# Optimization experiments

Measured on AMD Instinct MI355X. Metric: run time of the kernel, lower is better.

Reference implementation:

```python
import jax, jax.numpy as jnp
import numpy as np

KNN = 5
SEARCH = 3
CUTOFF = 1.0
NCLASSES = 21
D, H, W = 32, 128, 2048
P = 1048576


def setup_inputs() -> dict:
    key = jax.random.key(0)
    k1, k2, k3, k4, k5, k6 = jax.random.split(key, 6)
    proj_range = jax.random.uniform(k1, (D, H, W), dtype=jnp.float32)
    unproj_range = jax.random.uniform(k2, (P,), dtype=jnp.float32)
    proj_argmax = jax.random.randint(k3, (D, H, W), 0, NCLASSES).astype(jnp.int32)
    px = jax.random.randint(k4, (P,), 0, W).astype(jnp.int32)
    py = jax.random.randint(k5, (P,), 0, H).astype(jnp.int32)
    pz = jax.random.randint(k6, (P,), 0, D).astype(jnp.int32)
    return {"proj_range": proj_range, "unproj_range": unproj_range,
            "proj_argmax": proj_argmax, "px": px, "py": py, "pz": pz}


def reference(proj_range, unproj_range, proj_argmax, px, py, pz):
    pad = (SEARCH - 1) // 2
    k3 = SEARCH ** 3
    center = (k3 - 1) // 2  # = 13 for search=3
    n_pts = unproj_range.shape[0]

    # zero padding replicates F.unfold's implicit zero pad (padded entries stay 0,
    # which is NOT mapped to inf by the `< 0` mask, matching the torch code)
    pr_pad = jnp.pad(proj_range, pad)
    pa_pad = jnp.pad(proj_argmax, pad)

    # kernel offsets, flattened in (dz, dy, dx) order like unfoldNd
    offs = jnp.arange(SEARCH, dtype=jnp.int32)
    oz, oy, ox = jnp.meshgrid(offs, offs, offs, indexing="ij")
    oz, oy, ox = oz.reshape(-1), oy.reshape(-1), ox.reshape(-1)  # [k3]

    # per-point neighborhood indices into the padded volume: [P, k3]
    zi = pz[:, None] + oz[None, :]
    yi = py[:, None] + oy[None, :]
    xi = px[:, None] + ox[None, :]

    nb_rang = pr_pad[zi, yi, xi]                       # [P, k3]
    nb_rang = jnp.where(nb_rang < 0, jnp.inf, nb_rang)
    nb_rang = nb_rang.at[:, center].set(unproj_range)  # center = query range

    k2_dist = jnp.abs(nb_rang - unproj_range[:, None])  # [P, k3]

    neg_top, knn_idx = jax.lax.top_k(-k2_dist, KNN)     # smallest-k distances
    knn_dist = -neg_top                                  # [P, KNN]

    nb_arg = pa_pad[zi, yi, xi]                          # [P, k3] int
    knn_arg = jnp.take_along_axis(nb_arg, knn_idx, axis=1)
    knn_arg = jnp.where(knn_dist > CUTOFF, NCLASSES, knn_arg)  # cutoff -> invalid class

    # scatter-add voting over classes 0..NCLASSES
    counts = jnp.zeros((n_pts, NCLASSES + 1), dtype=proj_range.dtype)
    counts = counts.at[jnp.arange(n_pts, dtype=jnp.int32)[:, None], knn_arg].add(1.0)

    # argmax over classes 1..NCLASSES-1 (drop class 0 and invalid bucket), then +1
    out = jnp.argmax(counts[:, 1:-1], axis=1).astype(jnp.int32) + 1
    return out
```

## Files before the change

### kernel.cpp

```cpp
#include <hip/hip_runtime.h>
#include <hip/hip_bf16.h>
#include <math.h>

#define KNN 5
#define K3 27
#define CENTER 13
#define NCLASSES 21
#define DIM_D 32
#define DIM_H 128
#define DIM_W 2048

#define RADIX 256
#define BIN_PTS 2048
#define BIN_THREADS 256

__device__ __forceinline__ unsigned key16(int x, int y, int z) {
    return ((unsigned)z << 11) | ((unsigned)y << 4) | ((unsigned)x >> 7);
}

__global__ __launch_bounds__(256) void hist0_kernel(
    const int* __restrict__ px, const int* __restrict__ py,
    unsigned* __restrict__ h0, int P)
{
    __shared__ unsigned lh0[RADIX];
    int t = threadIdx.x;
    lh0[t] = 0;
    __syncthreads();
    int base4 = blockIdx.x * 1024 + t;
#pragma unroll
    for (int g = 0; g < 4; ++g) {
        int i4 = base4 + g * 256;
        int i0 = i4 * 4;
        if (i0 + 3 < P) {
            int4 X = ((const int4*)px)[i4];
            int4 Y = ((const int4*)py)[i4];
            atomicAdd(&lh0[(((unsigned)Y.x & 0xF) << 4) | ((unsigned)X.x >> 7)], 1u);
            atomicAdd(&lh0[(((unsigned)Y.y & 0xF) << 4) | ((unsigned)X.y >> 7)], 1u);
            atomicAdd(&lh0[(((unsigned)Y.z & 0xF) << 4) | ((unsigned)X.z >> 7)], 1u);
            atomicAdd(&lh0[(((unsigned)Y.w & 0xF) << 4) | ((unsigned)X.w >> 7)], 1u);
        } else {
            for (int i = i0; i < P; ++i)
                atomicAdd(&lh0[(((unsigned)py[i] & 0xF) << 4) | ((unsigned)px[i] >> 7)], 1u);
        }
    }
    __syncthreads();
    if (lh0[t]) atomicAdd(&h0[t], lh0[t]);
}

__global__ __launch_bounds__(256) void scan256_kernel(unsigned* __restrict__ h)
{
    __shared__ unsigned ws[4];
    int t = threadIdx.x, lane = t & 63, wid = t >> 6;
    unsigned a = h[t], ia = a;
#pragma unroll
    for (int off = 1; off < 64; off <<= 1) {
        unsigned v = __shfl_up(ia, off);
        if (lane >= off) ia += v;
    }
    if (lane == 63) ws[wid] = ia;
    __syncthreads();
    unsigned b = 0;
#pragma unroll
    for (int w = 0; w < 4; ++w) b += (w < wid) ? ws[w] : 0u;
    h[t] = b + ia - a;
}

struct BinShared {
    unsigned lh[RADIX];
    unsigned lscan[RADIX];
    unsigned gbase[RADIX];
    unsigned wsum[4];
    uint4 stage[BIN_PTS];
};

__device__ __forceinline__ void bin_local_scan(BinShared& S, int t)
{
    int lane = t & 63, wid = t >> 6;
    unsigned c = S.lh[t];
    unsigned inc = c;
#pragma unroll
    for (int off = 1; off < 64; off <<= 1) {
        unsigned v = __shfl_up(inc, off);
        if (lane >= off) inc += v;
    }
    if (lane == 63) S.wsum[wid] = inc;
    __syncthreads();
    unsigned wb = 0;
#pragma unroll
    for (int w = 0; w < 4; ++w) wb += (w < wid) ? S.wsum[w] : 0u;
    S.lscan[t] = wb + inc - c;
}

__global__ __launch_bounds__(BIN_THREADS) void bin_pass1_kernel(
    const float* __restrict__ ur, const int* __restrict__ px,
    const int* __restrict__ py, const int* __restrict__ pz,
    unsigned* __restrict__ g0, uint4* __restrict__ outp, int P)
{
    __shared__ BinShared S;
    int t = threadIdx.x;
    int bstart = blockIdx.x * BIN_PTS;
    int n = min(BIN_PTS, P - bstart);
    S.lh[t] = 0;
    __syncthreads();

    uint4 pay[8];
    unsigned rk[8], dg[8];
#pragma unroll
    for (int g = 0; g < 2; ++g) {
        int i4 = (bstart >> 2) + g * 256 + t;
        int i0 = i4 * 4;
        if (i0 + 3 < P) {
            int4 X = ((const int4*)px)[i4];
            int4 Y = ((const int4*)py)[i4];
            int4 Z = ((const int4*)pz)[i4];
            float4 U = ((const float4*)ur)[i4];
            int xs[4] = {X.x, X.y, X.z, X.w};
            int ys[4] = {Y.x, Y.y, Y.z, Y.w};
            int zs[4] = {Z.x, Z.y, Z.z, Z.w};
            float us[4] = {U.x, U.y, U.z, U.w};
#pragma unroll
            for (int c = 0; c < 4; ++c) {
                int j = g * 4 + c;
                unsigned k = key16(xs[c], ys[c], zs[c]);
                dg[j] = k & 0xFFu;
                rk[j] = atomicAdd(&S.lh[dg[j]], 1u);
                pay[j] = make_uint4(__float_as_uint(us[c]),
                    (unsigned)xs[c] | ((unsigned)ys[c] << 11) | ((unsigned)zs[c] << 18),
                    (unsigned)(i0 + c), 0u);
            }
        } else {
#pragma unroll
            for (int c = 0; c < 4; ++c) {
                int j = g * 4 + c;
                int gi = i0 + c;
                if (gi < P) {
                    int x = px[gi], y = py[gi], z = pz[gi];
                    unsigned k = key16(x, y, z);
                    dg[j] = k & 0xFFu;
                    rk[j] = atomicAdd(&S.lh[dg[j]], 1u);
                    pay[j] = make_uint4(__float_as_uint(ur[gi]),
                        (unsigned)x | ((unsigned)y << 11) | ((unsigned)z << 18),
                        (unsigned)gi, 0u);
                } else {
                    dg[j] = 0xFFFFFFFFu;
                }
            }
        }
    }
    __syncthreads();
    bin_local_scan(S, t);
    S.gbase[t] = S.lh[t] ? atomicAdd(&g0[t], S.lh[t]) : 0u;
    __syncthreads();
#pragma unroll
    for (int j = 0; j < 8; ++j)
        if (dg[j] != 0xFFFFFFFFu)
            S.stage[S.lscan[dg[j]] + rk[j]] = pay[j];
    __syncthreads();
#pragma unroll
    for (int j = 0; j < 8; ++j) {
        int s = j * 256 + t;
        if (s < n) {
            uint4 v = S.stage[s];
            unsigned d = (v.y >> 7) & 0xFFu;
            unsigned pos = S.gbase[d] + ((unsigned)s - S.lscan[d]);
            outp[pos] = v;
        }
    }
}

__global__ __launch_bounds__(BIN_THREADS) void hist_p2_kernel(
    const uint4* __restrict__ inp, unsigned* __restrict__ M,
    int gridB, int P)
{
    __shared__ unsigned lh[RADIX];
    int t = threadIdx.x;
    lh[t] = 0;
    __syncthreads();
    int bstart = blockIdx.x * BIN_PTS;
#pragma unroll
    for (int j = 0; j < 8; ++j) {
        int i = bstart + j * 256 + t;
        if (i < P) {
            uint4 v = inp[i];
            atomicAdd(&lh[(v.y >> 15) & 0xFFu], 1u);
        }
    }
    __syncthreads();
    M[(unsigned)t * (unsigned)gridB + blockIdx.x] = lh[t];
}

__global__ __launch_bounds__(1024) void scan_digit_kernel(
    unsigned* __restrict__ M, unsigned* __restrict__ T, int gridB)
{
    __shared__ unsigned wsum[16];
    unsigned* row = M + (size_t)blockIdx.x * (unsigned)gridB;
    int t = threadIdx.x, lane = t & 63, wid = t >> 6;
    int C = (gridB + 1023) / 1024;
    int lo = t * C, hi = min(lo + C, gridB);

    unsigned s = 0;
    for (int i = lo; i < hi; ++i) s += row[i];
    unsigned incl = s;
#pragma unroll
    for (int off = 1; off < 64; off <<= 1) {
        unsigned v = __shfl_up(incl, off);
        if (lane >= off) incl += v;
    }
    if (lane == 63) wsum[wid] = incl;
    __syncthreads();
    if (wid == 0 && lane < 16) {
        unsigned v = wsum[lane], iv = v;
#pragma unroll
        for (int off = 1; off < 16; off <<= 1) {
            unsigned u = __shfl_up(iv, off);
            if (lane >= off) iv += u;
        }
        wsum[lane] = iv - v;
    }
    __syncthreads();
    unsigned run = wsum[wid] + (incl - s);
    for (int i = lo; i < hi; ++i) {
        unsigned v = row[i];
        row[i] = run;
        run += v;
    }
    if (t == 1023) T[blockIdx.x] = run;
}

__global__ __launch_bounds__(BIN_THREADS) void bin_pass2_stable_kernel(
    const uint4* __restrict__ inp, const unsigned* __restrict__ M,
    const unsigned* __restrict__ T, uint4* __restrict__ outp,
    int gridB, int P)
{
    __shared__ BinShared S;
    int t = threadIdx.x;
    int bstart = blockIdx.x * BIN_PTS;
    int n = min(BIN_PTS, P - bstart);
    S.lh[t] = 0;
    __syncthreads();

    uint4 pay[8];
    unsigned rk[8], dg[8];
#pragma unroll
    for (int j = 0; j < 8; ++j) {
        int i = bstart + j * 256 + t;
        if (i < P) {
            uint4 v = inp[i];
            pay[j] = v;
            dg[j] = (v.y >> 15) & 0xFFu;
            rk[j] = atomicAdd(&S.lh[dg[j]], 1u);
        } else {
            dg[j] = 0xFFFFFFFFu;
        }
    }
    __syncthreads();
    bin_local_scan(S, t);
    S.gbase[t] = T[t] + M[(unsigned)t * (unsigned)gridB + blockIdx.x];
    __syncthreads();
#pragma unroll
    for (int j = 0; j < 8; ++j)
        if (dg[j] != 0xFFFFFFFFu)
            S.stage[S.lscan[dg[j]] + rk[j]] = pay[j];
    __syncthreads();
#pragma unroll
    for (int j = 0; j < 8; ++j) {
        int s = j * 256 + t;
        if (s < n) {
            uint4 v = S.stage[s];
            unsigned d = (v.y >> 15) & 0xFFu;
            unsigned pos = S.gbase[d] + ((unsigned)s - S.lscan[d]);
            outp[pos] = v;
        }
    }
}

__device__ __forceinline__ void bev_knn_body(
    const float* __restrict__ pr, const int* __restrict__ pa,
    float u, int x, int y, int z, int oidx, int* __restrict__ out)
{
    float dist[K3];
#pragma unroll
    for (int k = 0; k < K3; ++k) {
        const int dz = k / 9 - 1;
        const int dy = (k / 3) % 3 - 1;
        const int dx = k % 3 - 1;
        int zz = z + dz, yy = y + dy, xx = x + dx;
        bool ok = ((unsigned)zz < (unsigned)DIM_D) &
                  ((unsigned)yy < (unsigned)DIM_H) &
                  ((unsigned)xx < (unsigned)DIM_W);
        int zi = ok ? zz : 0;
        int yi = ok ? yy : 0;
        int xi = ok ? xx : 0;
        float r = pr[((size_t)zi * DIM_H + yi) * DIM_W + xi];
        r = ok ? r : 0.0f;
        r = (r < 0.0f) ? INFINITY : r;
        float d = fabsf(r - u);
        dist[k] = (k == CENTER) ? 0.0f : d;
    }

    float bd[KNN];
    int   bk[KNN];
#pragma unroll
    for (int j = 0; j < KNN; ++j) { bd[j] = INFINITY; bk[j] = -1; }
#pragma unroll
    for (int k = 0; k < K3; ++k) {
        float dcur = dist[k];
        int   kcur = k;
#pragma unroll
        for (int j = 0; j < KNN; ++j) {
            bool take = dcur < bd[j];
            float td = bd[j]; int tk = bk[j];
            bd[j] = take ? dcur : bd[j];
            bk[j] = take ? kcur : bk[j];
            dcur  = take ? td : dcur;
            kcur  = take ? tk : kcur;
        }
    }

    int votes[KNN];
#pragma unroll
    for (int j = 0; j < KNN; ++j) {
        int k = bk[j];
        const int dz = k / 9 - 1;
        const int dy = (k / 3) % 3 - 1;
        const int dx = k % 3 - 1;
        int zz = z + dz, yy = y + dy, xx = x + dx;
        bool ok = ((unsigned)zz < (unsigned)DIM_D) &
                  ((unsigned)yy < (unsigned)DIM_H) &
                  ((unsigned)xx < (unsigned)DIM_W);
        int zi = ok ? zz : 0;
        int yi = ok ? yy : 0;
        int xi = ok ? xx : 0;
        int cls = pa[((size_t)zi * DIM_H + yi) * DIM_W + xi];
        cls = ok ? cls : 0;
        cls = (bd[j] > 1.0f) ? NCLASSES : cls;
        votes[j] = cls;
    }

    int best_cnt = 0, best_cls = 1;
#pragma unroll
    for (int j = 0; j < KNN; ++j) {
        int v = votes[j];
        if (v >= 1 && v <= NCLASSES - 1) {
            int cnt = 0;
#pragma unroll
            for (int i = 0; i < KNN; ++i) cnt += (votes[i] == v) ? 1 : 0;
            if (cnt > best_cnt || (cnt == best_cnt && v < best_cls)) {
                best_cnt = cnt;
                best_cls = v;
            }
        }
    }
    out[oidx] = best_cls;
}

__device__ __forceinline__ int swizzle_block(int b, int nb) {
    if ((nb & 7) == 0) {
        int per = nb >> 3;
        return (b & 7) * per + (b >> 3);
    }
    return b;
}

__global__ __launch_bounds__(256) void bev_knn_aos_kernel(
    const float* __restrict__ pr, const int* __restrict__ pa,
    const uint4* __restrict__ payload, int* __restrict__ out, int P)
{
    int lb = swizzle_block(blockIdx.x, gridDim.x);
    int p = lb * blockDim.x + threadIdx.x;
    if (p >= P) return;
    uint4 w = payload[p];
    float u = __uint_as_float(w.x);
    int x = (int)(w.y & 0x7FFu);
    int y = (int)((w.y >> 11) & 0x7Fu);
    int z = (int)((w.y >> 18) & 0x1Fu);
    bev_knn_body(pr, pa, u, x, y, z, (int)w.z, out);
}

__global__ __launch_bounds__(256) void bev_knn_direct_kernel(
    const float* __restrict__ pr, const int* __restrict__ pa,
    const float* __restrict__ ur, const int* __restrict__ px,
    const int* __restrict__ py, const int* __restrict__ pz,
    int* __restrict__ out, int P)
{
    int p = blockIdx.x * blockDim.x + threadIdx.x;
    if (p >= P) return;
    bev_knn_body(pr, pa, ur[p], px[p], py[p], pz[p], p, out);
}

extern "C" void kernel_launch(void* const* d_in, const int* in_sizes, int n_in,
                              void* d_out, int out_size, void* d_ws, size_t ws_size,
                              hipStream_t stream) {
    const float* pr = (const float*)d_in[0];
    const float* ur = (const float*)d_in[1];
    const int*   pa = (const int*)d_in[2];
    const int*   px = (const int*)d_in[3];
    const int*   py = (const int*)d_in[4];
    const int*   pz = (const int*)d_in[5];
    int* out = (int*)d_out;
    int P = in_sizes[1];
    int block = 256;
    int grid = (P + block - 1) / block;
    int gridH = (P + 4095) / 4096;
    int gridB = (P + BIN_PTS - 1) / BIN_PTS;

    size_t h_b   = (size_t)RADIX * 4;
    size_t t_b   = (size_t)RADIX * 4;
    size_t m_b   = (size_t)RADIX * (size_t)gridB * 4;
    size_t m_off = (h_b + t_b + m_b + 15) & ~(size_t)15;
    size_t pay_b = (size_t)P * 16;
    size_t need_stable = m_off + 2 * pay_b;

    if (ws_size >= need_stable) {
        char* ws = (char*)d_ws;
        unsigned* h0   = (unsigned*)ws;
        unsigned* T    = (unsigned*)(ws + h_b);
        unsigned* M    = (unsigned*)(ws + h_b + t_b);
        uint4*    pay1 = (uint4*)(ws + m_off);
        uint4*    pay2 = (uint4*)(ws + m_off + pay_b);

        hipMemsetAsync(h0, 0, h_b, stream);
        hist0_kernel<<<gridH, 256, 0, stream>>>(px, py, h0, P);
        scan256_kernel<<<1, 256, 0, stream>>>(h0);
        bin_pass1_kernel<<<gridB, BIN_THREADS, 0, stream>>>(ur, px, py, pz,
                                                            h0, pay1, P);
        hist_p2_kernel<<<gridB, BIN_THREADS, 0, stream>>>(pay1, M, gridB, P);
        scan_digit_kernel<<<RADIX, 1024, 0, stream>>>(M, T, gridB);
        scan256_kernel<<<1, 256, 0, stream>>>(T);
        bin_pass2_stable_kernel<<<gridB, BIN_THREADS, 0, stream>>>(
            pay1, M, T, pay2, gridB, P);
        bev_knn_aos_kernel<<<grid, block, 0, stream>>>(pr, pa, pay2, out, P);
    } else {
        bev_knn_direct_kernel<<<grid, block, 0, stream>>>(pr, pa, ur, px, py,
                                                          pz, out, P);
    }
}
```

Before: 203.1 us.

## Fuse pass-2 histogram into pass-1 scatter and process two points per thread

Drops the separate hist_p2 kernel. Pass 1 now builds the second-digit per-block histogram M directly with global atomics keyed by destination block (pos>>11), and M is zeroed by an enlarged memset. The KNN kernel is also rewritten to handle two points per thread, interleaving their 27 gathers to raise memory-level parallelism, with half as many blocks. The costs are global atomic contention on M and higher register pressure from doubling per-thread state.

```diff
diff --git a/kernel.cpp b/kernel.cpp
--- a/kernel.cpp
+++ b/kernel.cpp
@@ -94,7 +94,8 @@
 __global__ __launch_bounds__(BIN_THREADS) void bin_pass1_kernel(
     const float* __restrict__ ur, const int* __restrict__ px,
     const int* __restrict__ py, const int* __restrict__ pz,
-    unsigned* __restrict__ g0, uint4* __restrict__ outp, int P)
+    unsigned* __restrict__ g0, uint4* __restrict__ outp,
+    unsigned* __restrict__ M, int gridB, int P)
 {
     __shared__ BinShared S;
     int t = threadIdx.x;
@@ -164,29 +165,10 @@
             unsigned d = (v.y >> 7) & 0xFFu;
             unsigned pos = S.gbase[d] + ((unsigned)s - S.lscan[d]);
             outp[pos] = v;
-        }
-    }
-}
-
-__global__ __launch_bounds__(BIN_THREADS) void hist_p2_kernel(
-    const uint4* __restrict__ inp, unsigned* __restrict__ M,
-    int gridB, int P)
-{
-    __shared__ unsigned lh[RADIX];
-    int t = threadIdx.x;
-    lh[t] = 0;
-    __syncthreads();
-    int bstart = blockIdx.x * BIN_PTS;
-#pragma unroll
-    for (int j = 0; j < 8; ++j) {
-        int i = bstart + j * 256 + t;
-        if (i < P) {
-            uint4 v = inp[i];
-            atomicAdd(&lh[(v.y >> 15) & 0xFFu], 1u);
-        }
-    }
-    __syncthreads();
-    M[(unsigned)t * (unsigned)gridB + blockIdx.x] = lh[t];
+            unsigned d1 = (v.y >> 15) & 0xFFu;
+            atomicAdd(&M[d1 * (unsigned)gridB + (pos >> 11)], 1u);
+        }
+    }
 }
 
 __global__ __launch_bounds__(1024) void scan_digit_kernel(
@@ -274,10 +256,134 @@
     }
 }
 
-__device__ __forceinline__ void bev_knn_body(
+__device__ __forceinline__ int swizzle_block(int b, int nb) {
+    if ((nb & 7) == 0) {
+        int per = nb >> 3;
+        return (b & 7) * per + (b >> 3);
+    }
+    return b;
+}
+
+__global__ __launch_bounds__(256) void bev_knn_aos2_kernel(
     const float* __restrict__ pr, const int* __restrict__ pa,
-    float u, int x, int y, int z, int oidx, int* __restrict__ out)
-{
+    const uint4* __restrict__ payload, int* __restrict__ out, int P)
+{
+    int lb = swizzle_block(blockIdx.x, gridDim.x);
+    int t = threadIdx.x;
+    int idx[2] = { lb * 512 + t, lb * 512 + 256 + t };
+
+    bool act[2];
+    float u[2];
+    int x[2], y[2], z[2], oidx[2];
+#pragma unroll
+    for (int q = 0; q < 2; ++q) {
+        act[q] = idx[q] < P;
+        uint4 w = payload[act[q] ? idx[q] : 0];
+        u[q] = __uint_as_float(w.x);
+        x[q] = (int)(w.y & 0x7FFu);
+        y[q] = (int)((w.y >> 11) & 0x7Fu);
+        z[q] = (int)((w.y >> 18) & 0x1Fu);
+        oidx[q] = (int)w.z;
+    }
+
+    float dist[2][K3];
+#pragma unroll
+    for (int k = 0; k < K3; ++k) {
+        const int dz = k / 9 - 1;
+        const int dy = (k / 3) % 3 - 1;
+        const int dx = k % 3 - 1;
+#pragma unroll
+        for (int q = 0; q < 2; ++q) {
+            int zz = z[q] + dz, yy = y[q] + dy, xx = x[q] + dx;
+            bool ok = ((unsigned)zz < (unsigned)DIM_D) &
+                      ((unsigned)yy < (unsigned)DIM_H) &
+                      ((unsigned)xx < (unsigned)DIM_W);
+            int zi = ok ? zz : 0;
+            int yi = ok ? yy : 0;
+            int xi = ok ? xx : 0;
+            float r = pr[((size_t)zi * DIM_H + yi) * DIM_W + xi];
+            r = ok ? r : 0.0f;
+            r = (r < 0.0f) ? INFINITY : r;
+            float d = fabsf(r - u[q]);
+            dist[q][k] = (k == CENTER) ? 0.0f : d;
+        }
+    }
+
+    float bd[2][KNN];
+    int   bk[2][KNN];
+#pragma unroll
+    for (int q = 0; q < 2; ++q) {
+#pragma unroll
+        for (int j = 0; j < KNN; ++j) { bd[q][j] = INFINITY; bk[q][j] = -1; }
+#pragma unroll
+        for (int k = 0; k < K3; ++k) {
+            float dcur = dist[q][k];
+            int   kcur = k;
+#pragma unroll
+            for (int j = 0; j < KNN; ++j) {
+                bool take = dcur < bd[q][j];
+                float td = bd[q][j]; int tk = bk[q][j];
+                bd[q][j] = take ? dcur : bd[q][j];
+                bk[q][j] = take ? kcur : bk[q][j];
+                dcur = take ? td : dcur;
+                kcur = take ? tk : kcur;
+            }
+        }
+    }
+
+    int votes[2][KNN];
+#pragma unroll
+    for (int j = 0; j < KNN; ++j) {
+#pragma unroll
+        for (int q = 0; q < 2; ++q) {
+            int k = bk[q][j];
+            const int dz = k / 9 - 1;
+            const int dy = (k / 3) % 3 - 1;
+            const int dx = k % 3 - 1;
+            int zz = z[q] + dz, yy = y[q] + dy, xx = x[q] + dx;
+            bool ok = ((unsigned)zz < (unsigned)DIM_D) &
+                      ((unsigned)yy < (unsigned)DIM_H) &
+                      ((unsigned)xx < (unsigned)DIM_W);
+            int zi = ok ? zz : 0;
+            int yi = ok ? yy : 0;
+            int xi = ok ? xx : 0;
+            int cls = pa[((size_t)zi * DIM_H + yi) * DIM_W + xi];
+            cls = ok ? cls : 0;
+            cls = (bd[q][j] > 1.0f) ? NCLASSES : cls;
+            votes[q][j] = cls;
+        }
+    }
+
+#pragma unroll
+    for (int q = 0; q < 2; ++q) {
+        int best_cnt = 0, best_cls = 1;
+#pragma unroll
+        for (int j = 0; j < KNN; ++j) {
+            int v = votes[q][j];
+            if (v >= 1 && v <= NCLASSES - 1) {
+                int cnt = 0;
+#pragma unroll
+                for (int i = 0; i < KNN; ++i) cnt += (votes[q][i] == v) ? 1 : 0;
+                if (cnt > best_cnt || (cnt == best_cnt && v < best_cls)) {
+                    best_cnt = cnt;
+                    best_cls = v;
+                }
+            }
+        }
+        if (act[q]) out[oidx[q]] = best_cls;
+    }
+}
+
+__global__ __launch_bounds__(256) void bev_knn_direct_kernel(
+    const float* __restrict__ pr, const int* __restrict__ pa,
+    const float* __restrict__ ur, const int* __restrict__ px,
+    const int* __restrict__ py, const int* __restrict__ pz,
+    int* __restrict__ out, int P)
+{
+    int p = blockIdx.x * blockDim.x + threadIdx.x;
+    if (p >= P) return;
+    float u = ur[p];
+    int x = px[p], y = py[p], z = pz[p];
     float dist[K3];
 #pragma unroll
     for (int k = 0; k < K3; ++k) {
@@ -297,26 +403,22 @@
         float d = fabsf(r - u);
         dist[k] = (k == CENTER) ? 0.0f : d;
     }
-
-    float bd[KNN];
-    int   bk[KNN];
+    float bd[KNN]; int bk[KNN];
 #pragma unroll
     for (int j = 0; j < KNN; ++j) { bd[j] = INFINITY; bk[j] = -1; }
 #pragma unroll
     for (int k = 0; k < K3; ++k) {
-        float dcur = dist[k];
-        int   kcur = k;
+        float dcur = dist[k]; int kcur = k;
 #pragma unroll
         for (int j = 0; j < KNN; ++j) {
             bool take = dcur < bd[j];
             float td = bd[j]; int tk = bk[j];
             bd[j] = take ? dcur : bd[j];
             bk[j] = take ? kcur : bk[j];
-            dcur  = take ? td : dcur;
-            kcur  = take ? tk : kcur;
-        }
-    }
-
+            dcur = take ? td : dcur;
+            kcur = take ? tk : kcur;
+        }
+    }
     int votes[KNN];
 #pragma unroll
     for (int j = 0; j < KNN; ++j) {
@@ -336,7 +438,6 @@
         cls = (bd[j] > 1.0f) ? NCLASSES : cls;
         votes[j] = cls;
     }
-
     int best_cnt = 0, best_cls = 1;
 #pragma unroll
     for (int j = 0; j < KNN; ++j) {
@@ -346,46 +447,11 @@
 #pragma unroll
             for (int i = 0; i < KNN; ++i) cnt += (votes[i] == v) ? 1 : 0;
             if (cnt > best_cnt || (cnt == best_cnt && v < best_cls)) {
-                best_cnt = cnt;
-                best_cls = v;
+                best_cnt = cnt; best_cls = v;
             }
         }
     }
-    out[oidx] = best_cls;
-}
-
-__device__ __forceinline__ int swizzle_block(int b, int nb) {
-    if ((nb & 7) == 0) {
-        int per = nb >> 3;
-        return (b & 7) * per + (b >> 3);
-    }
-    return b;
-}
-
-__global__ __launch_bounds__(256) void bev_knn_aos_kernel(
-    const float* __restrict__ pr, const int* __restrict__ pa,
-    const uint4* __restrict__ payload, int* __restrict__ out, int P)
-{
-    int lb = swizzle_block(blockIdx.x, gridDim.x);
-    int p = lb * blockDim.x + threadIdx.x;
-    if (p >= P) return;
-    uint4 w = payload[p];
-    float u = __uint_as_float(w.x);
-    int x = (int)(w.y & 0x7FFu);
-    int y = (int)((w.y >> 11) & 0x7Fu);
-    int z = (int)((w.y >> 18) & 0x1Fu);
-    bev_knn_body(pr, pa, u, x, y, z, (int)w.z, out);
-}
-
-__global__ __launch_bounds__(256) void bev_knn_direct_kernel(
-    const float* __restrict__ pr, const int* __restrict__ pa,
-    const float* __restrict__ ur, const int* __restrict__ px,
-    const int* __restrict__ py, const int* __restrict__ pz,
-    int* __restrict__ out, int P)
-{
-    int p = blockIdx.x * blockDim.x + threadIdx.x;
-    if (p >= P) return;
-    bev_knn_body(pr, pa, ur[p], px[p], py[p], pz[p], p, out);
+    out[p] = best_cls;
 }
 
 extern "C" void kernel_launch(void* const* d_in, const int* in_sizes, int n_in,
@@ -399,10 +465,9 @@
     const int*   pz = (const int*)d_in[5];
     int* out = (int*)d_out;
     int P = in_sizes[1];
-    int block = 256;
-    int grid = (P + block - 1) / block;
     int gridH = (P + 4095) / 4096;
     int gridB = (P + BIN_PTS - 1) / BIN_PTS;
+    int gridM = (P + 511) / 512;
 
     size_t h_b   = (size_t)RADIX * 4;
     size_t t_b   = (size_t)RADIX * 4;
@@ -419,19 +484,19 @@
         uint4*    pay1 = (uint4*)(ws + m_off);
         uint4*    pay2 = (uint4*)(ws + m_off + pay_b);
 
-        hipMemsetAsync(h0, 0, h_b, stream);
+        hipMemsetAsync(ws, 0, h_b + t_b + m_b, stream);
         hist0_kernel<<<gridH, 256, 0, stream>>>(px, py, h0, P);
         scan256_kernel<<<1, 256, 0, stream>>>(h0);
-        bin_pass1_kernel<<<gridB, BIN_THREADS, 0, stream>>>(ur, px, py, pz,
-                                                            h0, pay1, P);
-        hist_p2_kernel<<<gridB, BIN_THREADS, 0, stream>>>(pay1, M, gridB, P);
+        bin_pass1_kernel<<<gridB, BIN_THREADS, 0, stream>>>(
+            ur, px, py, pz, h0, pay1, M, gridB, P);
         scan_digit_kernel<<<RADIX, 1024, 0, stream>>>(M, T, gridB);
         scan256_kernel<<<1, 256, 0, stream>>>(T);
         bin_pass2_stable_kernel<<<gridB, BIN_THREADS, 0, stream>>>(
             pay1, M, T, pay2, gridB, P);
-        bev_knn_aos_kernel<<<grid, block, 0, stream>>>(pr, pa, pay2, out, P);
+        bev_knn_aos2_kernel<<<gridM, 256, 0, stream>>>(pr, pa, pay2, out, P);
     } else {
-        bev_knn_direct_kernel<<<grid, block, 0, stream>>>(pr, pa, ur, px, py,
-                                                          pz, out, P);
-    }
-}
+        int grid = (P + 255) / 256;
+        bev_knn_direct_kernel<<<grid, 256, 0, stream>>>(pr, pa, ur, px, py,
+                                                        pz, out, P);
+    }
+}
```

Result: slower. 246.2 us (+21.2%).

## Bucket points by (y, x-half, z) segments and stage neighborhood rows in LDS

Applied to the files above, without the earlier changes.

The radix binning now uses segment keys of y plus the x half for its first pass. A per-segment z counting sort replaces the global second-pass histogram, scan and stable scatter, which cuts several kernel launches. The KNN kernel gets one block per (z, y, x-half) segment. Each block loads the 9 neighboring 1024-wide rows of range and packed byte class into LDS, then processes its points from shared memory instead of scattered global gathers. The cost is large per-block LDS use (about 46 KB), uneven work per block, and a pass2 launch of only 256 blocks that loops over whole segments.

```diff
diff --git a/kernel.cpp b/kernel.cpp
--- a/kernel.cpp
+++ b/kernel.cpp
@@ -13,9 +13,16 @@
 #define RADIX 256
 #define BIN_PTS 2048
 #define BIN_THREADS 256
-
-__device__ __forceinline__ unsigned key16(int x, int y, int z) {
-    return ((unsigned)z << 11) | ((unsigned)y << 4) | ((unsigned)x >> 7);
+#define NG 8192
+#define ROWW 1032
+#define SEG_TILE 2048
+
+
+__device__ __forceinline__ unsigned seg_of_xy(int x, int y) {
+    return ((unsigned)y << 1) | ((unsigned)x >> 10);
+}
+__device__ __forceinline__ unsigned seg_of_wy(unsigned wy) {
+    return (((wy >> 11) & 0x7Fu) << 1) | ((wy >> 10) & 1u);
 }
 
 __global__ __launch_bounds__(256) void hist0_kernel(
@@ -34,20 +41,21 @@
         if (i0 + 3 < P) {
             int4 X = ((const int4*)px)[i4];
             int4 Y = ((const int4*)py)[i4];
-            atomicAdd(&lh0[(((unsigned)Y.x & 0xF) << 4) | ((unsigned)X.x >> 7)], 1u);
-            atomicAdd(&lh0[(((unsigned)Y.y & 0xF) << 4) | ((unsigned)X.y >> 7)], 1u);
-            atomicAdd(&lh0[(((unsigned)Y.z & 0xF) << 4) | ((unsigned)X.z >> 7)], 1u);
-            atomicAdd(&lh0[(((unsigned)Y.w & 0xF) << 4) | ((unsigned)X.w >> 7)], 1u);
+            atomicAdd(&lh0[seg_of_xy(X.x, Y.x)], 1u);
+            atomicAdd(&lh0[seg_of_xy(X.y, Y.y)], 1u);
+            atomicAdd(&lh0[seg_of_xy(X.z, Y.z)], 1u);
+            atomicAdd(&lh0[seg_of_xy(X.w, Y.w)], 1u);
         } else {
             for (int i = i0; i < P; ++i)
-                atomicAdd(&lh0[(((unsigned)py[i] & 0xF) << 4) | ((unsigned)px[i] >> 7)], 1u);
+                atomicAdd(&lh0[seg_of_xy(px[i], py[i])], 1u);
         }
     }
     __syncthreads();
     if (lh0[t]) atomicAdd(&h0[t], lh0[t]);
 }
 
-__global__ __launch_bounds__(256) void scan256_kernel(unsigned* __restrict__ h)
+__global__ __launch_bounds__(256) void scan256_dup_kernel(
+    unsigned* __restrict__ h, unsigned* __restrict__ hbase)
 {
     __shared__ unsigned ws[4];
     int t = threadIdx.x, lane = t & 63, wid = t >> 6;
@@ -62,7 +70,9 @@
     unsigned b = 0;
 #pragma unroll
     for (int w = 0; w < 4; ++w) b += (w < wid) ? ws[w] : 0u;
-    h[t] = b + ia - a;
+    unsigned excl = b + ia - a;
+    h[t] = excl;
+    hbase[t] = excl;
 }
 
 struct BinShared {
@@ -121,8 +131,7 @@
 #pragma unroll
             for (int c = 0; c < 4; ++c) {
                 int j = g * 4 + c;
-                unsigned k = key16(xs[c], ys[c], zs[c]);
-                dg[j] = k & 0xFFu;
+                dg[j] = seg_of_xy(xs[c], ys[c]);
                 rk[j] = atomicAdd(&S.lh[dg[j]], 1u);
                 pay[j] = make_uint4(__float_as_uint(us[c]),
                     (unsigned)xs[c] | ((unsigned)ys[c] << 11) | ((unsigned)zs[c] << 18),
@@ -135,8 +144,7 @@
                 int gi = i0 + c;
                 if (gi < P) {
                     int x = px[gi], y = py[gi], z = pz[gi];
-                    unsigned k = key16(x, y, z);
-                    dg[j] = k & 0xFFu;
+                    dg[j] = seg_of_xy(x, y);
                     rk[j] = atomicAdd(&S.lh[dg[j]], 1u);
                     pay[j] = make_uint4(__float_as_uint(ur[gi]),
                         (unsigned)x | ((unsigned)y << 11) | ((unsigned)z << 18),
@@ -161,123 +169,225 @@
         int s = j * 256 + t;
         if (s < n) {
             uint4 v = S.stage[s];
-            unsigned d = (v.y >> 7) & 0xFFu;
+            unsigned d = seg_of_wy(v.y);
             unsigned pos = S.gbase[d] + ((unsigned)s - S.lscan[d]);
             outp[pos] = v;
         }
     }
 }
 
-__global__ __launch_bounds__(BIN_THREADS) void hist_p2_kernel(
-    const uint4* __restrict__ inp, unsigned* __restrict__ M,
-    int gridB, int P)
-{
-    __shared__ unsigned lh[RADIX];
+__global__ __launch_bounds__(256) void pass2z_kernel(
+    const uint4* __restrict__ inp, const unsigned* __restrict__ segBase,
+    uint4* __restrict__ outp, unsigned* __restrict__ st, int P)
+{
+    __shared__ unsigned zh[32];
+    __shared__ unsigned cur[32];
+    __shared__ unsigned lz[32];
+    __shared__ unsigned lsc[32];
+    __shared__ uint4 stage[SEG_TILE];
+
+    int b = blockIdx.x;
+    unsigned s0 = segBase[b];
+    unsigned s1 = (b == RADIX - 1) ? (unsigned)P : segBase[b + 1];
     int t = threadIdx.x;
-    lh[t] = 0;
-    __syncthreads();
-    int bstart = blockIdx.x * BIN_PTS;
-#pragma unroll
-    for (int j = 0; j < 8; ++j) {
-        int i = bstart + j * 256 + t;
-        if (i < P) {
-            uint4 v = inp[i];
-            atomicAdd(&lh[(v.y >> 15) & 0xFFu], 1u);
-        }
-    }
-    __syncthreads();
-    M[(unsigned)t * (unsigned)gridB + blockIdx.x] = lh[t];
-}
-
-__global__ __launch_bounds__(1024) void scan_digit_kernel(
-    unsigned* __restrict__ M, unsigned* __restrict__ T, int gridB)
-{
-    __shared__ unsigned wsum[16];
-    unsigned* row = M + (size_t)blockIdx.x * (unsigned)gridB;
-    int t = threadIdx.x, lane = t & 63, wid = t >> 6;
-    int C = (gridB + 1023) / 1024;
-    int lo = t * C, hi = min(lo + C, gridB);
-
-    unsigned s = 0;
-    for (int i = lo; i < hi; ++i) s += row[i];
-    unsigned incl = s;
-#pragma unroll
-    for (int off = 1; off < 64; off <<= 1) {
-        unsigned v = __shfl_up(incl, off);
-        if (lane >= off) incl += v;
-    }
-    if (lane == 63) wsum[wid] = incl;
-    __syncthreads();
-    if (wid == 0 && lane < 16) {
-        unsigned v = wsum[lane], iv = v;
-#pragma unroll
-        for (int off = 1; off < 16; off <<= 1) {
+
+    if (t < 32) zh[t] = 0;
+    __syncthreads();
+
+    for (unsigned i = s0 + t; i < s1; i += 256)
+        atomicAdd(&zh[(inp[i].y >> 18) & 31u], 1u);
+    __syncthreads();
+
+    if (t < 64) {
+        unsigned v = (t < 32) ? zh[t] : 0u;
+        unsigned iv = v;
+#pragma unroll
+        for (int off = 1; off < 32; off <<= 1) {
             unsigned u = __shfl_up(iv, off);
-            if (lane >= off) iv += u;
-        }
-        wsum[lane] = iv - v;
-    }
-    __syncthreads();
-    unsigned run = wsum[wid] + (incl - s);
-    for (int i = lo; i < hi; ++i) {
-        unsigned v = row[i];
-        row[i] = run;
-        run += v;
-    }
-    if (t == 1023) T[blockIdx.x] = run;
-}
-
-__global__ __launch_bounds__(BIN_THREADS) void bin_pass2_stable_kernel(
-    const uint4* __restrict__ inp, const unsigned* __restrict__ M,
-    const unsigned* __restrict__ T, uint4* __restrict__ outp,
-    int gridB, int P)
-{
-    __shared__ BinShared S;
-    int t = threadIdx.x;
-    int bstart = blockIdx.x * BIN_PTS;
-    int n = min(BIN_PTS, P - bstart);
-    S.lh[t] = 0;
-    __syncthreads();
-
-    uint4 pay[8];
-    unsigned rk[8], dg[8];
-#pragma unroll
-    for (int j = 0; j < 8; ++j) {
-        int i = bstart + j * 256 + t;
-        if (i < P) {
-            uint4 v = inp[i];
-            pay[j] = v;
-            dg[j] = (v.y >> 15) & 0xFFu;
-            rk[j] = atomicAdd(&S.lh[dg[j]], 1u);
-        } else {
-            dg[j] = 0xFFFFFFFFu;
-        }
-    }
-    __syncthreads();
-    bin_local_scan(S, t);
-    S.gbase[t] = T[t] + M[(unsigned)t * (unsigned)gridB + blockIdx.x];
-    __syncthreads();
-#pragma unroll
-    for (int j = 0; j < 8; ++j)
-        if (dg[j] != 0xFFFFFFFFu)
-            S.stage[S.lscan[dg[j]] + rk[j]] = pay[j];
-    __syncthreads();
-#pragma unroll
-    for (int j = 0; j < 8; ++j) {
-        int s = j * 256 + t;
-        if (s < n) {
-            uint4 v = S.stage[s];
-            unsigned d = (v.y >> 15) & 0xFFu;
-            unsigned pos = S.gbase[d] + ((unsigned)s - S.lscan[d]);
-            outp[pos] = v;
-        }
-    }
-}
-
-__device__ __forceinline__ void bev_knn_body(
+            if (t >= off) iv += u;
+        }
+        if (t < 32) {
+            unsigned base = s0 + iv - v;
+            cur[t] = base;
+            st[b * 32 + t] = base;
+        }
+    }
+    __syncthreads();
+
+    for (unsigned tb = s0; tb < s1; tb += SEG_TILE) {
+        unsigned m = min((unsigned)SEG_TILE, s1 - tb);
+        if (t < 32) lz[t] = 0;
+        __syncthreads();
+        uint4 pay[8];
+        unsigned rk[8], zz[8];
+#pragma unroll
+        for (int j = 0; j < 8; ++j) {
+            int s = j * 256 + t;
+            if (s < (int)m) {
+                uint4 v = inp[tb + (unsigned)s];
+                pay[j] = v;
+                zz[j] = (v.y >> 18) & 31u;
+                rk[j] = atomicAdd(&lz[zz[j]], 1u);
+            } else {
+                zz[j] = 0xFFFFFFFFu;
+            }
+        }
+        __syncthreads();
+        if (t < 64) {
+            unsigned v = (t < 32) ? lz[t] : 0u;
+            unsigned iv = v;
+#pragma unroll
+            for (int off = 1; off < 32; off <<= 1) {
+                unsigned u = __shfl_up(iv, off);
+                if (t >= off) iv += u;
+            }
+            if (t < 32) lsc[t] = iv - v;
+        }
+        __syncthreads();
+#pragma unroll
+        for (int j = 0; j < 8; ++j)
+            if (zz[j] != 0xFFFFFFFFu)
+                stage[lsc[zz[j]] + rk[j]] = pay[j];
+        __syncthreads();
+#pragma unroll
+        for (int j = 0; j < 8; ++j) {
+            int s = j * 256 + t;
+            if (s < (int)m) {
+                uint4 v = stage[s];
+                unsigned z = (v.y >> 18) & 31u;
+                outp[cur[z] + ((unsigned)s - lsc[z])] = v;
+            }
+        }
+        __syncthreads();
+        if (t < 32) cur[t] += lz[t];
+        __syncthreads();
+    }
+}
+
+__device__ __forceinline__ int swizzle_block(int b, int nb) {
+    if ((nb & 7) == 0) {
+        int per = nb >> 3;
+        return (b & 7) * per + (b >> 3);
+    }
+    return b;
+}
+
+__global__ __launch_bounds__(256) void bev_knn_lds_kernel(
     const float* __restrict__ pr, const int* __restrict__ pa,
-    float u, int x, int y, int z, int oidx, int* __restrict__ out)
-{
+    const uint4* __restrict__ payload, const unsigned* __restrict__ st,
+    int* __restrict__ out, int P)
+{
+    __shared__ float prs[9 * ROWW];
+    __shared__ unsigned char pas[9 * ROWW];
+
+    int lb = swizzle_block(blockIdx.x, gridDim.x);
+    unsigned start = st[lb];
+    unsigned end   = (lb == NG - 1) ? (unsigned)P : st[lb + 1];
+    int cnt = (int)end - (int)start;
+    if (cnt <= 0) return;
+
+    int y  = lb >> 6;
+    int x0 = ((lb >> 5) & 1) << 10;
+    int z  = lb & 31;
+    int t  = threadIdx.x;
+
+    for (int r = 0; r < 9; ++r) {
+        int gz = z + r / 3 - 1;
+        int gy = y + r % 3 - 1;
+        bool inb = ((unsigned)gz < (unsigned)DIM_D) &
+                   ((unsigned)gy < (unsigned)DIM_H);
+        size_t rb = ((size_t)(gz * DIM_H + gy) << 11) + x0;
+        float4 f = make_float4(0.f, 0.f, 0.f, 0.f);
+        unsigned pk = 0u;
+        if (inb) {
+            f = ((const float4*)(pr + rb))[t];
+            int4 a = ((const int4*)(pa + rb))[t];
+            pk = (unsigned)a.x | ((unsigned)a.y << 8) |
+                 ((unsigned)a.z << 16) | ((unsigned)a.w << 24);
+        }
+        ((float4*)(prs + r * ROWW + 4))[t] = f;
+        ((unsigned*)(pas + r * ROWW + 4))[t] = pk;
+        if (t == 0) {
+            bool okl = inb && (x0 > 0);
+            prs[r * ROWW + 3] = okl ? pr[rb - 1] : 0.f;
+            pas[r * ROWW + 3] = okl ? (unsigned char)pa[rb - 1] : (unsigned char)0;
+            bool okr = inb && (x0 + 1024 < DIM_W);
+            prs[r * ROWW + 1028] = okr ? pr[rb + 1024] : 0.f;
+            pas[r * ROWW + 1028] = okr ? (unsigned char)pa[rb + 1024] : (unsigned char)0;
+        }
+    }
+    __syncthreads();
+
+    for (int i = t; i < cnt; i += 256) {
+        uint4 w = payload[start + i];
+        float u = __uint_as_float(w.x);
+        int xi = (int)(w.y & 1023u) + 4;
+
+        float dist[K3];
+#pragma unroll
+        for (int k = 0; k < K3; ++k) {
+            float r = prs[(k / 3) * ROWW + xi + (k % 3) - 1];
+            r = (r < 0.0f) ? INFINITY : r;
+            float d = fabsf(r - u);
+            dist[k] = (k == CENTER) ? 0.0f : d;
+        }
+
+        float bd[KNN];
+        int   bk[KNN];
+#pragma unroll
+        for (int j = 0; j < KNN; ++j) { bd[j] = INFINITY; bk[j] = -1; }
+#pragma unroll
+        for (int k = 0; k < K3; ++k) {
+            float dcur = dist[k];
+            int   kcur = k;
+#pragma unroll
+            for (int j = 0; j < KNN; ++j) {
+                bool take = dcur < bd[j];
+                float td = bd[j]; int tk = bk[j];
+                bd[j] = take ? dcur : bd[j];
+                bk[j] = take ? kcur : bk[j];
+                dcur  = take ? td : dcur;
+                kcur  = take ? tk : kcur;
+            }
+        }
+
+        int votes[KNN];
+#pragma unroll
+        for (int j = 0; j < KNN; ++j) {
+            int k = bk[j];
+            int cls = (int)pas[(k / 3) * ROWW + xi + (k % 3) - 1];
+            cls = (bd[j] > 1.0f) ? NCLASSES : cls;
+            votes[j] = cls;
+        }
+
+        int best_cnt = 0, best_cls = 1;
+#pragma unroll
+        for (int j = 0; j < KNN; ++j) {
+            int v = votes[j];
+            if (v >= 1 && v <= NCLASSES - 1) {
+                int c2 = 0;
+#pragma unroll
+                for (int q = 0; q < KNN; ++q) c2 += (votes[q] == v) ? 1 : 0;
+                if (c2 > best_cnt || (c2 == best_cnt && v < best_cls)) {
+                    best_cnt = c2;
+                    best_cls = v;
+                }
+            }
+        }
+        out[w.z] = best_cls;
+    }
+}
+
+__global__ __launch_bounds__(256) void bev_knn_direct_kernel(
+    const float* __restrict__ pr, const int* __restrict__ pa,
+    const float* __restrict__ ur, const int* __restrict__ px,
+    const int* __restrict__ py, const int* __restrict__ pz,
+    int* __restrict__ out, int P)
+{
+    int p = blockIdx.x * blockDim.x + threadIdx.x;
+    if (p >= P) return;
+    float u = ur[p];
+    int x = px[p], y = py[p], z = pz[p];
     float dist[K3];
 #pragma unroll
     for (int k = 0; k < K3; ++k) {
@@ -297,26 +407,22 @@
         float d = fabsf(r - u);
         dist[k] = (k == CENTER) ? 0.0f : d;
     }
-
-    float bd[KNN];
-    int   bk[KNN];
+    float bd[KNN]; int bk[KNN];
 #pragma unroll
     for (int j = 0; j < KNN; ++j) { bd[j] = INFINITY; bk[j] = -1; }
 #pragma unroll
     for (int k = 0; k < K3; ++k) {
-        float dcur = dist[k];
-        int   kcur = k;
+        float dcur = dist[k]; int kcur = k;
 #pragma unroll
         for (int j = 0; j < KNN; ++j) {
             bool take = dcur < bd[j];
             float td = bd[j]; int tk = bk[j];
             bd[j] = take ? dcur : bd[j];
             bk[j] = take ? kcur : bk[j];
-            dcur  = take ? td : dcur;
-            kcur  = take ? tk : kcur;
-        }
-    }
-
+            dcur = take ? td : dcur;
+            kcur = take ? tk : kcur;
+        }
+    }
     int votes[KNN];
 #pragma unroll
     for (int j = 0; j < KNN; ++j) {
@@ -336,7 +442,6 @@
         cls = (bd[j] > 1.0f) ? NCLASSES : cls;
         votes[j] = cls;
     }
-
     int best_cnt = 0, best_cls = 1;
 #pragma unroll
     for (int j = 0; j < KNN; ++j) {
@@ -346,46 +451,11 @@
 #pragma unroll
             for (int i = 0; i < KNN; ++i) cnt += (votes[i] == v) ? 1 : 0;
             if (cnt > best_cnt || (cnt == best_cnt && v < best_cls)) {
-                best_cnt = cnt;
-                best_cls = v;
-            }
-        }
-    }
-    out[oidx] = best_cls;
-}
-
-__device__ __forceinline__ int swizzle_block(int b, int nb) {
-    if ((nb & 7) == 0) {
-        int per = nb >> 3;
-        return (b & 7) * per + (b >> 3);
-    }
-    return b;
-}
-
-__global__ __launch_bounds__(256) void bev_knn_aos_kernel(
-    const float* __restrict__ pr, const int* __restrict__ pa,
-    const uint4* __restrict__ payload, int* __restrict__ out, int P)
-{
-    int lb = swizzle_block(blockIdx.x, gridDim.x);
-    int p = lb * blockDim.x + threadIdx.x;
-    if (p >= P) return;
-    uint4 w = payload[p];
-    float u = __uint_as_float(w.x);
-    int x = (int)(w.y & 0x7FFu);
-    int y = (int)((w.y >> 11) & 0x7Fu);
-    int z = (int)((w.y >> 18) & 0x1Fu);
-    bev_knn_body(pr, pa, u, x, y, z, (int)w.z, out);
-}
-
-__global__ __launch_bounds__(256) void bev_knn_direct_kernel(
-    const float* __restrict__ pr, const int* __restrict__ pa,
-    const float* __restrict__ ur, const int* __restrict__ px,
-    const int* __restrict__ py, const int* __restrict__ pz,
-    int* __restrict__ out, int P)
-{
-    int p = blockIdx.x * blockDim.x + threadIdx.x;
-    if (p >= P) return;
-    bev_knn_body(pr, pa, ur[p], px[p], py[p], pz[p], p, out);
+                best_cnt = cnt; best_cls = v;
+            }
+        }
+    }
+    out[p] = best_cls;
 }
 
 extern "C" void kernel_launch(void* const* d_in, const int* in_sizes, int n_in,
@@ -399,39 +469,34 @@
     const int*   pz = (const int*)d_in[5];
     int* out = (int*)d_out;
     int P = in_sizes[1];
-    int block = 256;
-    int grid = (P + block - 1) / block;
     int gridH = (P + 4095) / 4096;
     int gridB = (P + BIN_PTS - 1) / BIN_PTS;
+    int gridD = (P + 255) / 256;
 
     size_t h_b   = (size_t)RADIX * 4;
-    size_t t_b   = (size_t)RADIX * 4;
-    size_t m_b   = (size_t)RADIX * (size_t)gridB * 4;
-    size_t m_off = (h_b + t_b + m_b + 15) & ~(size_t)15;
+    size_t hb_b  = (size_t)RADIX * 4;
+    size_t st_b  = (size_t)NG * 4;
+    size_t p_off = (h_b + hb_b + st_b + 15) & ~(size_t)15;
     size_t pay_b = (size_t)P * 16;
-    size_t need_stable = m_off + 2 * pay_b;
-
-    if (ws_size >= need_stable) {
+    size_t need  = p_off + 2 * pay_b;
+
+    if (ws_size >= need) {
         char* ws = (char*)d_ws;
-        unsigned* h0   = (unsigned*)ws;
-        unsigned* T    = (unsigned*)(ws + h_b);
-        unsigned* M    = (unsigned*)(ws + h_b + t_b);
-        uint4*    pay1 = (uint4*)(ws + m_off);
-        uint4*    pay2 = (uint4*)(ws + m_off + pay_b);
-
-        hipMemsetAsync(h0, 0, h_b, stream);
-        hist0_kernel<<<gridH, 256, 0, stream>>>(px, py, h0, P);
-        scan256_kernel<<<1, 256, 0, stream>>>(h0);
+        unsigned* h0cur  = (unsigned*)ws;
+        unsigned* h0base = (unsigned*)(ws + h_b);
+        unsigned* st     = (unsigned*)(ws + h_b + hb_b);
+        uint4*    pay1   = (uint4*)(ws + p_off);
+        uint4*    pay2   = (uint4*)(ws + p_off + pay_b);
+
+        hipMemsetAsync(h0cur, 0, h_b, stream);
+        hist0_kernel<<<gridH, 256, 0, stream>>>(px, py, h0cur, P);
+        scan256_dup_kernel<<<1, 256, 0, stream>>>(h0cur, h0base);
         bin_pass1_kernel<<<gridB, BIN_THREADS, 0, stream>>>(ur, px, py, pz,
-                                                            h0, pay1, P);
-        hist_p2_kernel<<<gridB, BIN_THREADS, 0, stream>>>(pay1, M, gridB, P);
-        scan_digit_kernel<<<RADIX, 1024, 0, stream>>>(M, T, gridB);
-        scan256_kernel<<<1, 256, 0, stream>>>(T);
-        bin_pass2_stable_kernel<<<gridB, BIN_THREADS, 0, stream>>>(
-            pay1, M, T, pay2, gridB, P);
-        bev_knn_aos_kernel<<<grid, block, 0, stream>>>(pr, pa, pay2, out, P);
+                                                            h0cur, pay1, P);
+        pass2z_kernel<<<RADIX, 256, 0, stream>>>(pay1, h0base, pay2, st, P);
+        bev_knn_lds_kernel<<<NG, 256, 0, stream>>>(pr, pa, pay2, st, out, P);
     } else {
-        bev_knn_direct_kernel<<<grid, block, 0, stream>>>(pr, pa, ur, px, py,
-                                                          pz, out, P);
-    }
-}
+        bev_knn_direct_kernel<<<gridD, 256, 0, stream>>>(pr, pa, ur, px, py,
+                                                         pz, out, P);
+    }
+}
```

After: 239.7 us. 18.0% more time.
